# Performance work log

Hardware: AMD Instinct MI355X
Metric: run time of the kernel (lower is better)

The kernel has to match this reference:

```python
import jax, jax.numpy as jnp
import numpy as np

B, NE, NMAX = 256, 90, 270
ZE = PE = GE = PPS = 32
NPROPS = 20
FP, SGE, LATH = 256, 64, 128
PIN = FP + SGE + LATH  # 448 = pred_inp_size = conv input (add_to_node)
C1, C2, H = 448, 256, 3
P1 = P2 = 512
EPS = 1e-5

PNAMES = ['sg_emb_table','lat_W1','lat_b1','lat_bn1_g','lat_bn1_b','lat_bn1_m','lat_bn1_v',
          'lat_W2','lat_b2','lat_bn2_g','lat_bn2_b','lat_bn2_m','lat_bn2_v',
          'z_emb_table','period_table','group_table','props','W_props','b_props','W_phys','b_phys',
          'gat1_W','gat1_as','gat1_ad','gat1_b','gat2_W','gat2_as','gat2_ad','gat2_b',
          'pW1','pb1','pbn1_g','pbn1_b','pbn1_m','pbn1_v',
          'pW2','pb2','pbn2_g','pbn2_b','pbn2_m','pbn2_v','pW3','pb3']

def _bn(x, g, b, m, v):
    return (x - m) * g / jnp.sqrt(v + EPS) + b

def _lrelu(x, s=0.2):
    return jnp.where(x >= 0, x, s * x)

def _gat(x, adj, W, a_s, a_d, bias):
    # PyG DenseGATConv: concat=False (mean over heads), dropout=0, negative_slope=0.2
    Bn, N, _ = x.shape
    h = (x @ W).reshape(Bn, N, H, -1)                      # [B,N,H,C]
    asrc = (h * a_s).sum(-1)                               # [B,N,H]
    adst = (h * a_d).sum(-1)
    alpha = asrc[:, None, :, :] + adst[:, :, None, :]      # [B,i,j,H]
    alpha = _lrelu(alpha, 0.2)
    adj_sl = jnp.maximum(adj, jnp.eye(N, dtype=adj.dtype))  # add self loops
    alpha = jnp.where(adj_sl[..., None] > 0, alpha, -jnp.inf)
    alpha = jax.nn.softmax(alpha, axis=2)                  # softmax over sources j
    out = jnp.einsum('bijh,bjhc->bihc', alpha, h)
    return out.mean(2) + bias                              # [B,N,C]

def _forward(comp, sg, lat, period_idx, group_idx, p):
    sg_x = p['sg_emb_table'][sg[:, 0]]                     # [B,SGE]
    # lattice MLP: (Linear -> BN -> LeakyReLU(True)==identity) x2
    h = _bn(lat @ p['lat_W1'] + p['lat_b1'], p['lat_bn1_g'], p['lat_bn1_b'], p['lat_bn1_m'], p['lat_bn1_v'])
    lat_x = _bn(h @ p['lat_W2'] + p['lat_b2'], p['lat_bn2_g'], p['lat_bn2_b'], p['lat_bn2_m'], p['lat_bn2_v'])
    # ragged -> dense batch: expand composition counts into dense node-type grid
    n_atoms = comp.sum(1)                                  # [B]
    cum = jnp.cumsum(comp, axis=1)                         # [B,NE]
    t = jnp.arange(NMAX)
    z = jax.vmap(lambda c: jnp.searchsorted(c, t, side='right'))(cum)  # [B,NMAX]
    mask = t[None, :] < n_atoms[:, None]                   # [B,NMAX] valid nodes
    z = jnp.where(mask, z, 0)
    # PhysEmbedding: z/period/group embeddings + projected properties -> final proj
    phys = jnp.concatenate([
        p['z_emb_table'][z],
        p['period_table'][period_idx[z]],
        p['group_table'][group_idx[z]],
        p['props'][z] @ p['W_props'] + p['b_props'],
    ], axis=-1)
    phys = phys @ p['W_phys'] + p['b_phys']                # [B,NMAX,FP]
    # add_to_node: cat graph-level lat/sg embeddings onto every node, then zero-pad
    node = jnp.concatenate([
        phys,
        jnp.broadcast_to(lat_x[:, None, :], (lat_x.shape[0], NMAX, LATH)),
        jnp.broadcast_to(sg_x[:, None, :], (sg_x.shape[0], NMAX, SGE)),
    ], axis=-1)
    node = node * mask[..., None].astype(node.dtype)       # to_dense_batch zero padding
    # per-graph dense block adjacency, zero diagonal (fill_diagonal_(0))
    adj = (mask[:, :, None] & mask[:, None, :]).astype(node.dtype)
    adj = adj * (1.0 - jnp.eye(NMAX, dtype=node.dtype))
    # GNNBlock: act = LeakyReLU(True) == identity (negative_slope=1)
    x1 = _gat(node, adj, p['gat1_W'], p['gat1_as'], p['gat1_ad'], p['gat1_b'])
    x2 = _gat(x1, adj, p['gat2_W'], p['gat2_as'], p['gat2_ad'], p['gat2_b'])
    comp_x = x2.sum(1)                                     # sum over ALL NMAX slots (incl. padding, as torch does)
    feat = jnp.concatenate([comp_x, sg_x, lat_x], axis=-1) # [B,PIN]
    # prediction head (eval: dropout off, BN running stats)
    h = _lrelu(_bn(feat @ p['pW1'] + p['pb1'], p['pbn1_g'], p['pbn1_b'], p['pbn1_m'], p['pbn1_v']))
    h = _lrelu(_bn(h @ p['pW2'] + p['pb2'], p['pbn2_g'], p['pbn2_b'], p['pbn2_m'], p['pbn2_v']))
    return h @ p['pW3'] + p['pb3']                         # [B,1]

def setup_inputs():
    key = jax.random.key(0)
    ks = iter(jax.random.split(key, 64))
    def nrm(shape, s=0.05):
        return jax.random.normal(next(ks), shape, dtype=jnp.float32) * s
    comp = jax.random.randint(next(ks), (B, NE), 0, 4, dtype=jnp.int32)
    comp = comp.at[0].set(3)  # graph 0 has exactly NMAX atoms -> data N_max == NMAX
    sg = jax.random.randint(next(ks), (B, 1), 0, 230)
    lat = jax.random.uniform(next(ks), (B, 6), dtype=jnp.float32)
    period_idx = jax.random.randint(next(ks), (NE,), 0, 8)
    group_idx = jax.random.randint(next(ks), (NE,), 0, 19)
    inp = dict(comp=comp, sg=sg, lat=lat, period_idx=period_idx, group_idx=group_idx)
    inp.update(
        sg_emb_table=nrm((230, SGE)),
        lat_W1=nrm((6, LATH)), lat_b1=nrm((LATH,)),
        lat_bn1_g=jnp.ones(LATH), lat_bn1_b=jnp.zeros(LATH), lat_bn1_m=jnp.zeros(LATH), lat_bn1_v=jnp.ones(LATH),
        lat_W2=nrm((LATH, LATH)), lat_b2=nrm((LATH,)),
        lat_bn2_g=jnp.ones(LATH), lat_bn2_b=jnp.zeros(LATH), lat_bn2_m=jnp.zeros(LATH), lat_bn2_v=jnp.ones(LATH),
        z_emb_table=nrm((NE, ZE)), period_table=nrm((8, PE)), group_table=nrm((19, GE)),
        props=nrm((NE, NPROPS), 0.1), W_props=nrm((NPROPS, PPS)), b_props=nrm((PPS,)),
        W_phys=nrm((ZE + PE + GE + PPS, FP)), b_phys=nrm((FP,)),
        gat1_W=nrm((PIN, H * C1)), gat1_as=nrm((H, C1)), gat1_ad=nrm((H, C1)), gat1_b=nrm((C1,)),
        gat2_W=nrm((C1, H * C2)), gat2_as=nrm((H, C2)), gat2_ad=nrm((H, C2)), gat2_b=nrm((C2,)),
        pW1=nrm((PIN, P1)), pb1=nrm((P1,)),
        pbn1_g=jnp.ones(P1), pbn1_b=jnp.zeros(P1), pbn1_m=jnp.zeros(P1), pbn1_v=jnp.ones(P1),
        pW2=nrm((P1, P2)), pb2=nrm((P2,)),
        pbn2_g=jnp.ones(P2), pbn2_b=jnp.zeros(P2), pbn2_m=jnp.zeros(P2), pbn2_v=jnp.ones(P2),
        pW3=nrm((P2, 1)), pb3=nrm((1,)),
    )
    return inp

def reference(comp, sg, lat, period_idx, group_idx,
              sg_emb_table, lat_W1, lat_b1, lat_bn1_g, lat_bn1_b, lat_bn1_m, lat_bn1_v,
              lat_W2, lat_b2, lat_bn2_g, lat_bn2_b, lat_bn2_m, lat_bn2_v,
              z_emb_table, period_table, group_table, props, W_props, b_props, W_phys, b_phys,
              gat1_W, gat1_as, gat1_ad, gat1_b, gat2_W, gat2_as, gat2_ad, gat2_b,
              pW1, pb1, pbn1_g, pbn1_b, pbn1_m, pbn1_v,
              pW2, pb2, pbn2_g, pbn2_b, pbn2_m, pbn2_v, pW3, pb3):
    vals = (sg_emb_table, lat_W1, lat_b1, lat_bn1_g, lat_bn1_b, lat_bn1_m, lat_bn1_v,
            lat_W2, lat_b2, lat_bn2_g, lat_bn2_b, lat_bn2_m, lat_bn2_v,
            z_emb_table, period_table, group_table, props, W_props, b_props, W_phys, b_phys,
            gat1_W, gat1_as, gat1_ad, gat1_b, gat2_W, gat2_as, gat2_ad, gat2_b,
            pW1, pb1, pbn1_g, pbn1_b, pbn1_m, pbn1_v,
            pW2, pb2, pbn2_g, pbn2_b, pbn2_m, pbn2_v, pW3, pb3)
    p = dict(zip(PNAMES, vals))
    return _forward(comp, sg, lat, period_idx, group_idx, p)
```

## Files before the change

### kernel.cpp

```cpp
#include <hip/hip_runtime.h>
#include <math.h>

#define BB 256
#define NEL 90
#define NMAX 270
#define C1 448
#define C2 256
#define PIN 448
#define LATH 128
#define SGE 64
#define P1 512
#define EPSB 1e-5f

typedef short shortx8 __attribute__((ext_vector_type(8)));
typedef float floatx4 __attribute__((ext_vector_type(4)));

__device__ __forceinline__ float bf2f(unsigned short u) {
  return __uint_as_float(((unsigned)u) << 16);
}
__device__ __forceinline__ unsigned short f2bf(float f) {
  unsigned x = __float_as_uint(f);
  unsigned r = (x + 0x7fffu + ((x >> 16) & 1u)) >> 16;
  return (unsigned short)r;
}
__device__ __forceinline__ void gld16(const void* g, void* l) {
  __builtin_amdgcn_global_load_lds(
      (const __attribute__((address_space(1))) unsigned int*)g,
      (__attribute__((address_space(3))) unsigned int*)l, 16, 0, 0);
}

__global__ __launch_bounds__(256) void k_prep(
    const int* __restrict__ comp, const int* __restrict__ sg, const float* __restrict__ lat,
    const float* __restrict__ sg_emb,
    const float* __restrict__ W1, const float* __restrict__ b1,
    const float* __restrict__ g1, const float* __restrict__ be1,
    const float* __restrict__ m1, const float* __restrict__ v1,
    const float* __restrict__ W2, const float* __restrict__ b2,
    const float* __restrict__ g2, const float* __restrict__ be2,
    const float* __restrict__ m2, const float* __restrict__ v2,
    float* __restrict__ sgx, float* __restrict__ latx,
    int* __restrict__ z, int* __restrict__ natoms) {
  int b = blockIdx.x;
  int tid = threadIdx.x;
  __shared__ int cum[NEL];
  __shared__ float hbuf[LATH];
  __shared__ float latl[6];
  if (tid == 0) {
    int s = 0;
    for (int e = 0; e < NEL; ++e) { s += comp[b * NEL + e]; cum[e] = s; }
    natoms[b] = s;
  }
  if (tid < 6) latl[tid] = lat[b * 6 + tid];
  __syncthreads();
  int n = cum[NEL - 1];
  for (int t = tid; t < NMAX; t += blockDim.x) {
    int zz = -1;
    if (t < n) {
      for (int e = 0; e < NEL; ++e) { if (cum[e] > t) { zz = e; break; } }
    }
    z[b * NMAX + t] = zz;
  }
  if (tid < SGE) {
    int si = sg[b];
    sgx[b * SGE + tid] = sg_emb[si * SGE + tid];
  }
  if (tid < LATH) {
    float acc = b1[tid];
    for (int k = 0; k < 6; ++k) acc += latl[k] * W1[k * LATH + tid];
    acc = (acc - m1[tid]) * g1[tid] * rsqrtf(v1[tid] + EPSB) + be1[tid];
    hbuf[tid] = acc;
  }
  __syncthreads();
  if (tid < LATH) {
    float acc = b2[tid];
    for (int k = 0; k < LATH; ++k) acc += hbuf[k] * W2[k * LATH + tid];
    acc = (acc - m2[tid]) * g2[tid] * rsqrtf(v2[tid] + EPSB) + be2[tid];
    latx[b * LATH + tid] = acc;
  }
}

__global__ __launch_bounds__(256) void k_scan(const int* __restrict__ natoms,
                                              int* __restrict__ off,
                                              int* __restrict__ aoff,
                                              float* __restrict__ zerobuf) {
  __shared__ int sh[BB];
  int tid = threadIdx.x;
  zerobuf[tid] = 0.f;
  int v0 = natoms[tid];
  sh[tid] = v0;
  for (int d = 1; d < BB; d <<= 1) {
    __syncthreads();
    int v = (tid >= d) ? sh[tid - d] : 0;
    __syncthreads();
    sh[tid] += v;
  }
  __syncthreads();
  off[tid] = sh[tid] - v0;
  __syncthreads();
  int sz = 3 * ((((v0 + 15) >> 4) << 4)) * ((((v0 + 31) >> 5) << 5));
  sh[tid] = sz;
  for (int d = 1; d < BB; d <<= 1) {
    __syncthreads();
    int v = (tid >= d) ? sh[tid - d] : 0;
    __syncthreads();
    sh[tid] += v;
  }
  __syncthreads();
  aoff[tid] = sh[tid] - sz;
}

__global__ __launch_bounds__(256) void k_physpe(
    const int* __restrict__ period_idx, const int* __restrict__ group_idx,
    const float* __restrict__ z_emb, const float* __restrict__ period_t,
    const float* __restrict__ group_t, const float* __restrict__ props,
    const float* __restrict__ Wp, const float* __restrict__ bp,
    const float* __restrict__ Wphys, const float* __restrict__ bphys,
    float* __restrict__ physpe) {
  int e = blockIdx.x;
  int tid = threadIdx.x;
  __shared__ float ph[128];
  if (tid < 32) ph[tid] = z_emb[e * 32 + tid];
  else if (tid < 64) ph[tid] = period_t[period_idx[e] * 32 + tid - 32];
  else if (tid < 96) ph[tid] = group_t[group_idx[e] * 32 + tid - 64];
  else if (tid < 128) {
    int j = tid - 96;
    float acc = bp[j];
    for (int k = 0; k < 20; ++k) acc += props[e * 20 + k] * Wp[k * 32 + j];
    ph[tid] = acc;
  }
  __syncthreads();
  float acc = bphys[tid];
  for (int k = 0; k < 128; ++k) acc += ph[k] * Wphys[k * 256 + tid];
  physpe[e * 256 + tid] = acc;
}

__global__ __launch_bounds__(256) void k_nodep(
    const int* __restrict__ z, const int* __restrict__ off, const int* __restrict__ natoms,
    const float* __restrict__ physpe, const float* __restrict__ latx,
    const float* __restrict__ sgx, unsigned short* __restrict__ x0) {
  int b = blockIdx.x;
  int n = natoms[b], ob = off[b];
  int tid = threadIdx.x;
  __shared__ int zl[NMAX];
  for (int t = tid; t < n; t += 256) zl[t] = z[b * NMAX + t];
  __syncthreads();
  int items = n * 56;
  for (int e = tid; e < items; e += 256) {
    int t = e / 56, c8 = (e - t * 56) << 3;
    int zt = zl[t];
    float v[8];
    if (c8 < 256) {
      float4 a = *(const float4*)(physpe + zt * 256 + c8);
      float4 c = *(const float4*)(physpe + zt * 256 + c8 + 4);
      v[0] = a.x; v[1] = a.y; v[2] = a.z; v[3] = a.w;
      v[4] = c.x; v[5] = c.y; v[6] = c.z; v[7] = c.w;
    } else if (c8 < 384) {
      float4 a = *(const float4*)(latx + b * LATH + c8 - 256);
      float4 c = *(const float4*)(latx + b * LATH + c8 - 252);
      v[0] = a.x; v[1] = a.y; v[2] = a.z; v[3] = a.w;
      v[4] = c.x; v[5] = c.y; v[6] = c.z; v[7] = c.w;
    } else {
      float4 a = *(const float4*)(sgx + b * SGE + c8 - 384);
      float4 c = *(const float4*)(sgx + b * SGE + c8 - 380);
      v[0] = a.x; v[1] = a.y; v[2] = a.z; v[3] = a.w;
      v[4] = c.x; v[5] = c.y; v[6] = c.z; v[7] = c.w;
    }
    unsigned short u[8];
    #pragma unroll
    for (int i = 0; i < 8; ++i) u[i] = f2bf(v[i]);
    *(uint4*)(x0 + (size_t)(ob + t) * PIN + c8) = *(uint4*)u;
  }
}

__global__ __launch_bounds__(256) void k_wprep(
    const float* __restrict__ W, unsigned short* __restrict__ Wt, int K, int NC3) {
  int k0 = blockIdx.x << 5;
  int c0 = blockIdx.y << 5;
  __shared__ float ts[32][33];
  int e = threadIdx.x << 2;
  int kk = e >> 5, cc = e & 31;
  float4 v = *(const float4*)(W + (size_t)(k0 + kk) * NC3 + c0 + cc);
  ts[kk][cc] = v.x; ts[kk][cc + 1] = v.y; ts[kk][cc + 2] = v.z; ts[kk][cc + 3] = v.w;
  __syncthreads();
  int c2 = threadIdx.x & 31, kg = threadIdx.x >> 5;
  ushort4 u;
  u.x = f2bf(ts[kg * 4 + 0][c2]); u.y = f2bf(ts[kg * 4 + 1][c2]);
  u.z = f2bf(ts[kg * 4 + 2][c2]); u.w = f2bf(ts[kg * 4 + 3][c2]);
  *(ushort4*)(Wt + (size_t)(c0 + c2) * K + k0 + (kg << 2)) = u;
}

__global__ __launch_bounds__(64) void k_fold(
    const float* __restrict__ W, const float* __restrict__ a_s, const float* __restrict__ a_d,
    int NC3, int C, float* __restrict__ wsv, float* __restrict__ wdv) {
  int k = blockIdx.x;
  int tid = threadIdx.x;
  for (int h = 0; h < 3; ++h) {
    float ss = 0.f, sd = 0.f;
    for (int c = tid; c < C; c += 64) {
      float wv = W[(size_t)k * NC3 + h * C + c];
      ss += wv * a_s[h * C + c];
      sd += wv * a_d[h * C + c];
    }
    for (int o = 32; o > 0; o >>= 1) { ss += __shfl_down(ss, o); sd += __shfl_down(sd, o); }
    if (tid == 0) { wsv[k * 3 + h] = ss; wdv[k * 3 + h] = sd; }
  }
}

__global__ __launch_bounds__(256) void k_av2(
    const unsigned short* __restrict__ x, const float* __restrict__ wsv,
    const float* __restrict__ wdv, const int* __restrict__ off,
    const int* __restrict__ natoms, float* __restrict__ asrc,
    float* __restrict__ adst, int K) {
  __shared__ float sw[C1 * 3], dw[C1 * 3];
  int tid = threadIdx.x;
  for (int e = tid; e < K * 3; e += 256) { sw[e] = wsv[e]; dw[e] = wdv[e]; }
  __syncthreads();
  int total = off[BB - 1] + natoms[BB - 1];
  int row = blockIdx.x * 256 + tid;
  if (row >= total) return;
  const unsigned short* xr = x + (size_t)row * K;
  float s0 = 0.f, s1 = 0.f, s2 = 0.f, d0 = 0.f, d1 = 0.f, d2 = 0.f;
  for (int k = 0; k < K; k += 8) {
    uint4 raw = *(const uint4*)(xr + k);
    unsigned short us[8];
    *(uint4*)us = raw;
    #pragma unroll
    for (int u = 0; u < 8; ++u) {
      float xv = bf2f(us[u]);
      int kb = (k + u) * 3;
      s0 += xv * sw[kb + 0]; s1 += xv * sw[kb + 1]; s2 += xv * sw[kb + 2];
      d0 += xv * dw[kb + 0]; d1 += xv * dw[kb + 1]; d2 += xv * dw[kb + 2];
    }
  }
  asrc[row * 3 + 0] = s0; asrc[row * 3 + 1] = s1; asrc[row * 3 + 2] = s2;
  adst[row * 3 + 0] = d0; adst[row * 3 + 1] = d1; adst[row * 3 + 2] = d2;
}

#define MTMAX 17
__global__ __launch_bounds__(256) void k_alpha(
    const float* __restrict__ asrc, const float* __restrict__ adst,
    const int* __restrict__ off, const int* __restrict__ natoms,
    const int* __restrict__ aoff, unsigned short* __restrict__ alpha) {
  int bid = blockIdx.x;
  int b = bid & (BB - 1);
  int hm = bid >> 8;
  int h = hm % 3;
  int mt = hm / 3;
  int n = natoms[b];
  if (n == 0) return;
  int mtn = (n + 15) >> 4;
  if (mt >= mtn) return;
  int ktn = (n + 31) >> 5;
  int rext = mtn << 4, kext = ktn << 5;
  int ob = off[b];
  size_t ab = (size_t)aoff[b] + (size_t)h * rext * kext;
  int tid = threadIdx.x;
  int wv = tid >> 6, lane = tid & 63;
  __shared__ float asl[288];
  for (int j = tid; j < kext; j += 256)
    asl[j] = (j < n) ? asrc[(ob + j) * 3 + h] : 0.f;
  __syncthreads();
  #pragma unroll
  for (int r = 0; r < 4; ++r) {
    int i = (mt << 4) + (wv << 2) + r;
    unsigned short* rowp = alpha + ab + (size_t)i * kext;
    if (i >= n) {
      for (int j = lane; j < kext; j += 64) rowp[j] = 0;
      continue;
    }
    float ad = adst[(ob + i) * 3 + h];
    float m = -1e30f;
    for (int j = lane; j < n; j += 64) {
      float sc = asl[j] + ad;
      sc = fmaxf(sc, 0.2f * sc);
      m = fmaxf(m, sc);
    }
    for (int o = 32; o > 0; o >>= 1) m = fmaxf(m, __shfl_xor(m, o));
    float s = 0.f;
    for (int j = lane; j < n; j += 64) {
      float sc = asl[j] + ad;
      sc = fmaxf(sc, 0.2f * sc);
      s += __expf(sc - m);
    }
    for (int o = 32; o > 0; o >>= 1) s += __shfl_xor(s, o);
    float rs = 1.f / s;
    for (int j = lane; j < kext; j += 64) {
      float v = 0.f;
      if (j < n) {
        float sc = asl[j] + ad;
        sc = fmaxf(sc, 0.2f * sc);
        v = __expf(sc - m) * rs;
      }
      rowp[j] = f2bf(v);
    }
  }
}

#define MTW 5

__global__ __launch_bounds__(256, 2) void k_fused_mfma(
    const unsigned short* __restrict__ xin, const unsigned short* __restrict__ Wt,
    const unsigned short* __restrict__ alpha, const int* __restrict__ aoff,
    const int* __restrict__ off, const int* __restrict__ natoms,
    const float* __restrict__ bias, const float* __restrict__ zerobuf,
    unsigned short* __restrict__ xout, int K, int C, int NC) {
  int bid = blockIdx.x;
  int xg = bid & 7;
  int g = bid >> 3;
  int cblk = g % NC;
  int b = xg + ((g / NC) << 3);
  int c0 = cblk << 6;
  int n = natoms[b];
  if (n == 0) return;
  int ob = off[b];
  size_t ab = (size_t)aoff[b];
  int tid = threadIdx.x;
  int wv = tid >> 6;
  int lane = tid & 63;
  int m16 = lane & 15;
  int q = lane >> 4;

  int mtn = (n + 15) >> 4;
  int jmax = mtn << 4;
  int ktn = (n + 31) >> 5;
  int kext = ktn << 5;
  size_t hstride = (size_t)jmax * kext;

  __shared__ unsigned short xs[2][17 * 512];
  __shared__ unsigned short tt[36 * 512];

  const unsigned short* xsrc[MTW];
  #pragma unroll
  for (int t_i = 0; t_i < MTW; ++t_i) {
    int mt = wv + (t_i << 2);
    int j = (mt << 4) + m16;
    xsrc[t_i] = (j < n) ? (xin + (size_t)(ob + j) * K + (q << 3))
                        : (const unsigned short*)zerobuf;
  }

  floatx4 acc[MTW][4];
  #pragma unroll
  for (int i = 0; i < MTW; ++i)
    #pragma unroll
    for (int nt = 0; nt < 4; ++nt) acc[i][nt] = (floatx4)0.f;

  for (int h = 0; h < 3; ++h) {
    floatx4 tac[MTW][4];
    #pragma unroll
    for (int i = 0; i < MTW; ++i)
      #pragma unroll
      for (int nt = 0; nt < 4; ++nt) tac[i][nt] = (floatx4)0.f;

    const unsigned short* wsrc = Wt + (size_t)(h * C + c0 + lane) * K + (wv << 3);

    #pragma unroll
    for (int t_i = 0; t_i < MTW; ++t_i) {
      int mt = wv + (t_i << 2);
      if (mt < mtn) gld16(xsrc[t_i], &xs[0][mt << 9]);
    }
    gld16(wsrc, &tt[wv << 9]);
    __syncthreads();

    int buf = 0;
    for (int k0 = 0; k0 < K; k0 += 32) {
      int k1 = k0 + 32;
      if (k1 < K) {
        #pragma unroll
        for (int t_i = 0; t_i < MTW; ++t_i) {
          int mt = wv + (t_i << 2);
          if (mt < mtn) gld16(xsrc[t_i] + k1, &xs[buf ^ 1][mt << 9]);
        }
        gld16(wsrc + k1, &tt[((buf ^ 1) << 11) + (wv << 9)]);
      }
      const unsigned short* wb = &tt[buf << 11];
      shortx8 bfr[4];
      #pragma unroll
      for (int nt = 0; nt < 4; ++nt)
        bfr[nt] = *(const shortx8*)(wb + (q << 9) + (((nt << 4) + m16) << 3));
      #pragma unroll
      for (int t_i = 0; t_i < MTW; ++t_i) {
        int mt = wv + (t_i << 2);
        if (mt < mtn) {
          shortx8 a = *(const shortx8*)(&xs[buf][(mt << 9) + (((q << 4) + m16) << 3)]);
          #pragma unroll
          for (int nt = 0; nt < 4; ++nt)
            tac[t_i][nt] = __builtin_amdgcn_mfma_f32_16x16x32_bf16(a, bfr[nt], tac[t_i][nt], 0, 0, 0);
        }
      }
      __syncthreads();
      buf ^= 1;
    }
    #pragma unroll
    for (int t_i = 0; t_i < MTW; ++t_i) {
      int mt = wv + (t_i << 2);
      if (mt < mtn) {
        int jbase = (mt << 4) + (q << 2);
        #pragma unroll
        for (int nt = 0; nt < 4; ++nt) {
          floatx4 d = tac[t_i][nt];
          ushort4 u;
          u.x = f2bf(d.x); u.y = f2bf(d.y); u.z = f2bf(d.z); u.w = f2bf(d.w);
          int c = (nt << 4) + m16;
          *(ushort4*)(tt + ((jbase >> 3) << 9) + (c << 3) + (jbase & 7)) = u;
        }
      }
    }
    for (int e = tid; e < ((kext - jmax) << 6); e += 256) {
      int j = jmax + (e >> 6), c = e & 63;
      tt[((j >> 3) << 9) + (c << 3) + (j & 7)] = 0;
    }
    __syncthreads();
    const unsigned short* ap = alpha + ab + (size_t)h * hstride;
    for (int k0p = 0; k0p < kext; k0p += 32) {
      shortx8 tb[4];
      #pragma unroll
      for (int nt = 0; nt < 4; ++nt)
        tb[nt] = *(const shortx8*)(tt + (((k0p >> 3) + q) << 9) + (((nt << 4) + m16) << 3));
      #pragma unroll
      for (int t_i = 0; t_i < MTW; ++t_i) {
        int mt = wv + (t_i << 2);
        if (mt < mtn) {
          shortx8 af = *(const shortx8*)(ap + (size_t)((mt << 4) + m16) * kext + k0p + (q << 3));
          #pragma unroll
          for (int nt = 0; nt < 4; ++nt)
            acc[t_i][nt] = __builtin_amdgcn_mfma_f32_16x16x32_bf16(af, tb[nt], acc[t_i][nt], 0, 0, 0);
        }
      }
    }
    __syncthreads();
  }
  float bq[4];
  #pragma unroll
  for (int nt = 0; nt < 4; ++nt) bq[nt] = bias[c0 + (nt << 4) + m16];
  const float inv3 = 1.f / 3.f;
  #pragma unroll
  for (int t_i = 0; t_i < MTW; ++t_i) {
    int mt = wv + (t_i << 2);
    if (mt < mtn) {
      #pragma unroll
      for (int nt = 0; nt < 4; ++nt) {
        floatx4 d = acc[t_i][nt];
        int cidx = c0 + (nt << 4) + m16;
        #pragma unroll
        for (int r = 0; r < 4; ++r) {
          int i = (mt << 4) + (q << 2) + r;
          if (i < n) xout[(size_t)(ob + i) * C + cidx] = f2bf(d[r] * inv3 + bq[nt]);
        }
      }
    }
  }
}

__global__ __launch_bounds__(128) void k_pad(
    const float* __restrict__ b1, const float* __restrict__ W2,
    const float* __restrict__ b2g, float* __restrict__ pad2) {
  int c = blockIdx.x;
  int tid = threadIdx.x;
  float s = 0.f;
  for (int k = tid; k < C1; k += 128) {
    float bv = b1[k];
    const float* wr = W2 + (size_t)k * (3 * C2) + c;
    s += bv * (wr[0] + wr[C2] + wr[2 * C2]);
  }
  __shared__ float red[128];
  red[tid] = s;
  __syncthreads();
  for (int st = 64; st > 0; st >>= 1) {
    if (tid < st) red[tid] += red[tid + st];
    __syncthreads();
  }
  if (tid == 0) pad2[c] = red[0] * (1.f / 3.f) + b2g[c];
}

__global__ __launch_bounds__(256) void k_feat2(
    const unsigned short* __restrict__ x2, const float* __restrict__ pad2,
    const int* __restrict__ off, const int* __restrict__ natoms,
    const float* __restrict__ sgx, const float* __restrict__ latx,
    float* __restrict__ feat) {
  int b = blockIdx.y;
  int chunk = blockIdx.x;
  int tid = threadIdx.x;
  int n = natoms[b], ob = off[b];
  if (chunk == 17) {
    atomicAdd(&feat[b * PIN + tid], (float)(NMAX - n) * pad2[tid]);
    if (tid < SGE) feat[b * PIN + 256 + tid] = sgx[b * SGE + tid];
    if (tid < LATH) feat[b * PIN + 320 + tid] = latx[b * LATH + tid];
    return;
  }
  int i0 = chunk << 4;
  if (i0 >= n) return;
  int i1 = min(i0 + 16, n);
  float s = 0.f;
  for (int i = i0; i < i1; ++i) s += bf2f(x2[(size_t)(ob + i) * C2 + tid]);
  atomicAdd(&feat[b * PIN + tid], s);
}

__global__ __launch_bounds__(512) void k_head(
    const float* __restrict__ feat,
    const float* __restrict__ W1, const float* __restrict__ b1,
    const float* __restrict__ g1, const float* __restrict__ be1,
    const float* __restrict__ m1, const float* __restrict__ v1,
    const float* __restrict__ W2, const float* __restrict__ b2,
    const float* __restrict__ g2, const float* __restrict__ be2,
    const float* __restrict__ m2, const float* __restrict__ v2,
    const float* __restrict__ W3, const float* __restrict__ b3,
    float* __restrict__ out) {
  int b = blockIdx.x, tid = threadIdx.x;
  __shared__ float f[PIN];
  __shared__ float h1[P1];
  __shared__ float h2[P1];
  __shared__ float red[512];
  for (int i = tid; i < PIN; i += 512) f[i] = feat[b * PIN + i];
  __syncthreads();
  {
    int o = tid;
    float acc = b1[o];
    for (int k = 0; k < PIN; ++k) acc += f[k] * W1[k * P1 + o];
    acc = (acc - m1[o]) * g1[o] * rsqrtf(v1[o] + EPSB) + be1[o];
    h1[o] = acc >= 0.f ? acc : 0.2f * acc;
  }
  __syncthreads();
  {
    int o = tid;
    float acc = b2[o];
    for (int k = 0; k < P1; ++k) acc += h1[k] * W2[k * P1 + o];
    acc = (acc - m2[o]) * g2[o] * rsqrtf(v2[o] + EPSB) + be2[o];
    h2[o] = acc >= 0.f ? acc : 0.2f * acc;
  }
  __syncthreads();
  red[tid] = h2[tid] * W3[tid];
  __syncthreads();
  for (int s = 256; s > 0; s >>= 1) {
    if (tid < s) red[tid] += red[tid + s];
    __syncthreads();
  }
  if (tid == 0) out[b] = red[0] + b3[0];
}

extern "C" void kernel_launch(void* const* d_in, const int* in_sizes, int n_in,
                              void* d_out, int out_size, void* d_ws, size_t ws_size,
                              hipStream_t stream) {
  const int*   comp       = (const int*)d_in[0];
  const int*   sg         = (const int*)d_in[1];
  const float* lat        = (const float*)d_in[2];
  const int*   period_idx = (const int*)d_in[3];
  const int*   group_idx  = (const int*)d_in[4];
  const float* sg_emb     = (const float*)d_in[5];
  const float* lat_W1     = (const float*)d_in[6];
  const float* lat_b1     = (const float*)d_in[7];
  const float* lat_bn1_g  = (const float*)d_in[8];
  const float* lat_bn1_b  = (const float*)d_in[9];
  const float* lat_bn1_m  = (const float*)d_in[10];
  const float* lat_bn1_v  = (const float*)d_in[11];
  const float* lat_W2     = (const float*)d_in[12];
  const float* lat_b2     = (const float*)d_in[13];
  const float* lat_bn2_g  = (const float*)d_in[14];
  const float* lat_bn2_b  = (const float*)d_in[15];
  const float* lat_bn2_m  = (const float*)d_in[16];
  const float* lat_bn2_v  = (const float*)d_in[17];
  const float* z_emb      = (const float*)d_in[18];
  const float* period_t   = (const float*)d_in[19];
  const float* group_t    = (const float*)d_in[20];
  const float* props      = (const float*)d_in[21];
  const float* W_props    = (const float*)d_in[22];
  const float* b_props    = (const float*)d_in[23];
  const float* W_phys     = (const float*)d_in[24];
  const float* b_phys     = (const float*)d_in[25];
  const float* gat1_W     = (const float*)d_in[26];
  const float* gat1_as    = (const float*)d_in[27];
  const float* gat1_ad    = (const float*)d_in[28];
  const float* gat1_b     = (const float*)d_in[29];
  const float* gat2_W     = (const float*)d_in[30];
  const float* gat2_as    = (const float*)d_in[31];
  const float* gat2_ad    = (const float*)d_in[32];
  const float* gat2_b     = (const float*)d_in[33];
  const float* pW1        = (const float*)d_in[34];
  const float* pb1        = (const float*)d_in[35];
  const float* pbn1_g     = (const float*)d_in[36];
  const float* pbn1_b     = (const float*)d_in[37];
  const float* pbn1_m     = (const float*)d_in[38];
  const float* pbn1_v     = (const float*)d_in[39];
  const float* pW2        = (const float*)d_in[40];
  const float* pb2        = (const float*)d_in[41];
  const float* pbn2_g     = (const float*)d_in[42];
  const float* pbn2_b     = (const float*)d_in[43];
  const float* pbn2_m     = (const float*)d_in[44];
  const float* pbn2_v     = (const float*)d_in[45];
  const float* pW3        = (const float*)d_in[46];
  const float* pb3        = (const float*)d_in[47];

  float* ws = (float*)d_ws;
  const size_t o_sgx  = 0;
  const size_t o_latx = o_sgx  + (size_t)BB * SGE;
  const size_t o_nat  = o_latx + (size_t)BB * LATH;
  const size_t o_off  = o_nat  + BB;
  const size_t o_aoff = o_off  + BB;
  const size_t o_z    = o_aoff + BB;
  const size_t o_phys = o_z    + (size_t)BB * NMAX;
  const size_t o_wsv  = o_phys + (size_t)NEL * 256;
  const size_t o_wdv  = o_wsv  + (size_t)C1 * 3;
  const size_t o_asrc = o_wdv  + (size_t)C1 * 3;
  const size_t o_adst = o_asrc + (size_t)BB * NMAX * 3;
  const size_t o_pad2 = o_adst + (size_t)BB * NMAX * 3;
  const size_t o_zero = o_pad2 + 256;
  const size_t o_wt1  = o_zero + 256;
  const size_t o_wt2  = o_wt1  + (size_t)(3 * C1) * PIN / 2;
  const size_t o_x0   = o_wt2  + (size_t)(3 * C2) * C1 / 2;
  const size_t o_x1   = o_x0   + (size_t)BB * NMAX * PIN / 2;
  const size_t o_alph = o_x1   + (size_t)BB * NMAX * PIN / 2;

  float* sgx    = ws + o_sgx;
  float* latx   = ws + o_latx;
  int*   natoms = (int*)(ws + o_nat);
  int*   off    = (int*)(ws + o_off);
  int*   aoff   = (int*)(ws + o_aoff);
  int*   z      = (int*)(ws + o_z);
  float* physpe = ws + o_phys;
  float* wsv    = ws + o_wsv;
  float* wdv    = ws + o_wdv;
  float* asrc   = ws + o_asrc;
  float* adst   = ws + o_adst;
  float* pad2   = ws + o_pad2;
  float* zerobuf = ws + o_zero;
  unsigned short* wt1   = (unsigned short*)(ws + o_wt1);
  unsigned short* wt2   = (unsigned short*)(ws + o_wt2);
  unsigned short* x0    = (unsigned short*)(ws + o_x0);
  unsigned short* x1    = (unsigned short*)(ws + o_x1);
  unsigned short* x2    = x0;
  unsigned short* alpha = (unsigned short*)(ws + o_alph);
  float* feat   = ws + o_x1;

  const int AVG = (BB * NMAX + 255) / 256;
  const int ALG = BB * 3 * MTMAX;

  k_prep<<<BB, 256, 0, stream>>>(comp, sg, lat, sg_emb,
      lat_W1, lat_b1, lat_bn1_g, lat_bn1_b, lat_bn1_m, lat_bn1_v,
      lat_W2, lat_b2, lat_bn2_g, lat_bn2_b, lat_bn2_m, lat_bn2_v,
      sgx, latx, z, natoms);
  k_scan<<<1, 256, 0, stream>>>(natoms, off, aoff, zerobuf);
  k_physpe<<<NEL, 256, 0, stream>>>(period_idx, group_idx, z_emb, period_t, group_t,
      props, W_props, b_props, W_phys, b_phys, physpe);
  k_nodep<<<BB, 256, 0, stream>>>(z, off, natoms, physpe, latx, sgx, x0);

  k_wprep<<<dim3(PIN / 32, (3 * C1) / 32), 256, 0, stream>>>(gat1_W, wt1, PIN, 3 * C1);
  k_wprep<<<dim3(C1 / 32, (3 * C2) / 32), 256, 0, stream>>>(gat2_W, wt2, C1, 3 * C2);
  k_pad<<<256, 128, 0, stream>>>(gat1_b, gat2_W, gat2_b, pad2);

  k_fold<<<C1, 64, 0, stream>>>(gat1_W, gat1_as, gat1_ad, 3 * C1, C1, wsv, wdv);
  k_av2<<<AVG, 256, 0, stream>>>(x0, wsv, wdv, off, natoms, asrc, adst, PIN);
  k_alpha<<<ALG, 256, 0, stream>>>(asrc, adst, off, natoms, aoff, alpha);
  k_fused_mfma<<<(C1 / 64) * BB, 256, 0, stream>>>(x0, wt1, alpha, aoff,
      off, natoms, gat1_b, zerobuf, x1, PIN, C1, C1 / 64);

  k_fold<<<C1, 64, 0, stream>>>(gat2_W, gat2_as, gat2_ad, 3 * C2, C2, wsv, wdv);
  k_av2<<<AVG, 256, 0, stream>>>(x1, wsv, wdv, off, natoms, asrc, adst, C1);
  k_alpha<<<ALG, 256, 0, stream>>>(asrc, adst, off, natoms, aoff, alpha);
  k_fused_mfma<<<(C2 / 64) * BB, 256, 0, stream>>>(x1, wt2, alpha, aoff,
      off, natoms, gat2_b, zerobuf, x2, C1, C2, C2 / 64);

  hipMemsetAsync(feat, 0, (size_t)BB * PIN * sizeof(float), stream);
  k_feat2<<<dim3(18, BB), 256, 0, stream>>>(x2, pad2, off, natoms, sgx, latx, feat);
  k_head<<<BB, 512, 0, stream>>>(feat,
      pW1, pb1, pbn1_g, pbn1_b, pbn1_m, pbn1_v,
      pW2, pb2, pbn2_g, pbn2_b, pbn2_m, pbn2_v,
      pW3, pb3, (float*)d_out);
}
```

Baseline: 753.6 us.

## Halve GAT column tile and read GEMM operands directly from global memory

The fused GAT kernel now computes 32 output columns per block instead of 64, doubling the grid and shrinking the LDS transpose buffer. The first GEMM stage drops the double-buffered global-to-LDS staging and its per-step barriers, loading X rows and weight fragments straight into registers. Occupancy hint rises from 2 to 3 blocks per CU. The aim is more parallelism and fewer syncs, at the cost of more redundant global reads of X and alpha across column blocks and less load/compute overlap.

```diff
diff --git a/kernel.cpp b/kernel.cpp
--- a/kernel.cpp
+++ b/kernel.cpp
@@ -11,6 +11,7 @@
 #define SGE 64
 #define P1 512
 #define EPSB 1e-5f
+#define KDIM 448
 
 typedef short shortx8 __attribute__((ext_vector_type(8)));
 typedef float floatx4 __attribute__((ext_vector_type(4)));
@@ -22,11 +23,6 @@
   unsigned x = __float_as_uint(f);
   unsigned r = (x + 0x7fffu + ((x >> 16) & 1u)) >> 16;
   return (unsigned short)r;
-}
-__device__ __forceinline__ void gld16(const void* g, void* l) {
-  __builtin_amdgcn_global_load_lds(
-      (const __attribute__((address_space(1))) unsigned int*)g,
-      (__attribute__((address_space(3))) unsigned int*)l, 16, 0, 0);
 }
 
 __global__ __launch_bounds__(256) void k_prep(
@@ -298,18 +294,18 @@
 
 #define MTW 5
 
-__global__ __launch_bounds__(256, 2) void k_fused_mfma(
+__global__ __launch_bounds__(256, 3) void k_fused_mfma(
     const unsigned short* __restrict__ xin, const unsigned short* __restrict__ Wt,
     const unsigned short* __restrict__ alpha, const int* __restrict__ aoff,
     const int* __restrict__ off, const int* __restrict__ natoms,
     const float* __restrict__ bias, const float* __restrict__ zerobuf,
-    unsigned short* __restrict__ xout, int K, int C, int NC) {
+    unsigned short* __restrict__ xout, int C, int NC) {
   int bid = blockIdx.x;
   int xg = bid & 7;
   int g = bid >> 3;
   int cblk = g % NC;
   int b = xg + ((g / NC) << 3);
-  int c0 = cblk << 6;
+  int c0 = cblk << 5;
   int n = natoms[b];
   if (n == 0) return;
   int ob = off[b];
@@ -326,69 +322,42 @@
   int kext = ktn << 5;
   size_t hstride = (size_t)jmax * kext;
 
-  __shared__ unsigned short xs[2][17 * 512];
-  __shared__ unsigned short tt[36 * 512];
+  __shared__ unsigned short tt[36 * 256];
 
   const unsigned short* xsrc[MTW];
   #pragma unroll
   for (int t_i = 0; t_i < MTW; ++t_i) {
     int mt = wv + (t_i << 2);
     int j = (mt << 4) + m16;
-    xsrc[t_i] = (j < n) ? (xin + (size_t)(ob + j) * K + (q << 3))
+    xsrc[t_i] = (j < n) ? (xin + (size_t)(ob + j) * KDIM + (q << 3))
                         : (const unsigned short*)zerobuf;
   }
 
-  floatx4 acc[MTW][4];
+  floatx4 acc[MTW][2];
   #pragma unroll
-  for (int i = 0; i < MTW; ++i)
+  for (int i = 0; i < MTW; ++i) { acc[i][0] = (floatx4)0.f; acc[i][1] = (floatx4)0.f; }
+
+  for (int h = 0; h < 3; ++h) {
+    floatx4 tac[MTW][2];
     #pragma unroll
-    for (int nt = 0; nt < 4; ++nt) acc[i][nt] = (floatx4)0.f;
-
-  for (int h = 0; h < 3; ++h) {
-    floatx4 tac[MTW][4];
-    #pragma unroll
-    for (int i = 0; i < MTW; ++i)
-      #pragma unroll
-      for (int nt = 0; nt < 4; ++nt) tac[i][nt] = (floatx4)0.f;
-
-    const unsigned short* wsrc = Wt + (size_t)(h * C + c0 + lane) * K + (wv << 3);
-
-    #pragma unroll
-    for (int t_i = 0; t_i < MTW; ++t_i) {
-      int mt = wv + (t_i << 2);
-      if (mt < mtn) gld16(xsrc[t_i], &xs[0][mt << 9]);
-    }
-    gld16(wsrc, &tt[wv << 9]);
-    __syncthreads();
-
-    int buf = 0;
-    for (int k0 = 0; k0 < K; k0 += 32) {
-      int k1 = k0 + 32;
-      if (k1 < K) {
-        #pragma unroll
-        for (int t_i = 0; t_i < MTW; ++t_i) {
-          int mt = wv + (t_i << 2);
-          if (mt < mtn) gld16(xsrc[t_i] + k1, &xs[buf ^ 1][mt << 9]);
-        }
-        gld16(wsrc + k1, &tt[((buf ^ 1) << 11) + (wv << 9)]);
-      }
-      const unsigned short* wb = &tt[buf << 11];
-      shortx8 bfr[4];
-      #pragma unroll
-      for (int nt = 0; nt < 4; ++nt)
-        bfr[nt] = *(const shortx8*)(wb + (q << 9) + (((nt << 4) + m16) << 3));
+    for (int i = 0; i < MTW; ++i) { tac[i][0] = (floatx4)0.f; tac[i][1] = (floatx4)0.f; }
+
+    const unsigned short* wp0 = Wt + (size_t)(h * C + c0 + m16) * KDIM + (q << 3);
+    const unsigned short* wp1 = Wt + (size_t)(h * C + c0 + 16 + m16) * KDIM + (q << 3);
+
+    #pragma unroll 2
+    for (int k0 = 0; k0 < KDIM; k0 += 32) {
+      shortx8 b0 = *(const shortx8*)(wp0 + k0);
+      shortx8 b1 = *(const shortx8*)(wp1 + k0);
       #pragma unroll
       for (int t_i = 0; t_i < MTW; ++t_i) {
         int mt = wv + (t_i << 2);
         if (mt < mtn) {
-          shortx8 a = *(const shortx8*)(&xs[buf][(mt << 9) + (((q << 4) + m16) << 3)]);
-          #pragma unroll
-          for (int nt = 0; nt < 4; ++nt)
-            tac[t_i][nt] = __builtin_amdgcn_mfma_f32_16x16x32_bf16(a, bfr[nt], tac[t_i][nt], 0, 0, 0);
+          shortx8 a = *(const shortx8*)(xsrc[t_i] + k0);
+          tac[t_i][0] = __builtin_amdgcn_mfma_f32_16x16x32_bf16(a, b0, tac[t_i][0], 0, 0, 0);
+          tac[t_i][1] = __builtin_amdgcn_mfma_f32_16x16x32_bf16(a, b1, tac[t_i][1], 0, 0, 0);
         }
       }
-      __syncthreads();
-      buf ^= 1;
     }
     #pragma unroll
     for (int t_i = 0; t_i < MTW; ++t_i) {
@@ -396,55 +365,52 @@
       if (mt < mtn) {
         int jbase = (mt << 4) + (q << 2);
         #pragma unroll
-        for (int nt = 0; nt < 4; ++nt) {
+        for (int nt = 0; nt < 2; ++nt) {
           floatx4 d = tac[t_i][nt];
           ushort4 u;
           u.x = f2bf(d.x); u.y = f2bf(d.y); u.z = f2bf(d.z); u.w = f2bf(d.w);
           int c = (nt << 4) + m16;
-          *(ushort4*)(tt + ((jbase >> 3) << 9) + (c << 3) + (jbase & 7)) = u;
+          *(ushort4*)(tt + ((jbase >> 3) << 8) + (c << 3) + (jbase & 7)) = u;
         }
       }
     }
-    for (int e = tid; e < ((kext - jmax) << 6); e += 256) {
-      int j = jmax + (e >> 6), c = e & 63;
-      tt[((j >> 3) << 9) + (c << 3) + (j & 7)] = 0;
+    for (int e = tid; e < ((kext - jmax) << 5); e += 256) {
+      int j = jmax + (e >> 5), c = e & 31;
+      tt[((j >> 3) << 8) + (c << 3) + (j & 7)] = 0;
     }
     __syncthreads();
     const unsigned short* ap = alpha + ab + (size_t)h * hstride;
     for (int k0p = 0; k0p < kext; k0p += 32) {
-      shortx8 tb[4];
-      #pragma unroll
-      for (int nt = 0; nt < 4; ++nt)
-        tb[nt] = *(const shortx8*)(tt + (((k0p >> 3) + q) << 9) + (((nt << 4) + m16) << 3));
+      shortx8 tb0 = *(const shortx8*)(tt + (((k0p >> 3) + q) << 8) + (m16 << 3));
+      shortx8 tb1 = *(const shortx8*)(tt + (((k0p >> 3) + q) << 8) + ((16 + m16) << 3));
       #pragma unroll
       for (int t_i = 0; t_i < MTW; ++t_i) {
         int mt = wv + (t_i << 2);
         if (mt < mtn) {
           shortx8 af = *(const shortx8*)(ap + (size_t)((mt << 4) + m16) * kext + k0p + (q << 3));
-          #pragma unroll
-          for (int nt = 0; nt < 4; ++nt)
-            acc[t_i][nt] = __builtin_amdgcn_mfma_f32_16x16x32_bf16(af, tb[nt], acc[t_i][nt], 0, 0, 0);
+          acc[t_i][0] = __builtin_amdgcn_mfma_f32_16x16x32_bf16(af, tb0, acc[t_i][0], 0, 0, 0);
+          acc[t_i][1] = __builtin_amdgcn_mfma_f32_16x16x32_bf16(af, tb1, acc[t_i][1], 0, 0, 0);
         }
       }
     }
     __syncthreads();
   }
-  float bq[4];
-  #pragma unroll
-  for (int nt = 0; nt < 4; ++nt) bq[nt] = bias[c0 + (nt << 4) + m16];
+  float bq0 = bias[c0 + m16];
+  float bq1 = bias[c0 + 16 + m16];
   const float inv3 = 1.f / 3.f;
   #pragma unroll
   for (int t_i = 0; t_i < MTW; ++t_i) {
     int mt = wv + (t_i << 2);
     if (mt < mtn) {
       #pragma unroll
-      for (int nt = 0; nt < 4; ++nt) {
+      for (int nt = 0; nt < 2; ++nt) {
         floatx4 d = acc[t_i][nt];
+        float bq = nt ? bq1 : bq0;
         int cidx = c0 + (nt << 4) + m16;
         #pragma unroll
         for (int r = 0; r < 4; ++r) {
           int i = (mt << 4) + (q << 2) + r;
-          if (i < n) xout[(size_t)(ob + i) * C + cidx] = f2bf(d[r] * inv3 + bq[nt]);
+          if (i < n) xout[(size_t)(ob + i) * C + cidx] = f2bf(d[r] * inv3 + bq);
         }
       }
     }
@@ -649,14 +615,14 @@
   k_fold<<<C1, 64, 0, stream>>>(gat1_W, gat1_as, gat1_ad, 3 * C1, C1, wsv, wdv);
   k_av2<<<AVG, 256, 0, stream>>>(x0, wsv, wdv, off, natoms, asrc, adst, PIN);
   k_alpha<<<ALG, 256, 0, stream>>>(asrc, adst, off, natoms, aoff, alpha);
-  k_fused_mfma<<<(C1 / 64) * BB, 256, 0, stream>>>(x0, wt1, alpha, aoff,
-      off, natoms, gat1_b, zerobuf, x1, PIN, C1, C1 / 64);
+  k_fused_mfma<<<(C1 / 32) * BB, 256, 0, stream>>>(x0, wt1, alpha, aoff,
+      off, natoms, gat1_b, zerobuf, x1, C1, C1 / 32);
 
   k_fold<<<C1, 64, 0, stream>>>(gat2_W, gat2_as, gat2_ad, 3 * C2, C2, wsv, wdv);
   k_av2<<<AVG, 256, 0, stream>>>(x1, wsv, wdv, off, natoms, asrc, adst, C1);
   k_alpha<<<ALG, 256, 0, stream>>>(asrc, adst, off, natoms, aoff, alpha);
-  k_fused_mfma<<<(C2 / 64) * BB, 256, 0, stream>>>(x1, wt2, alpha, aoff,
-      off, natoms, gat2_b, zerobuf, x2, C1, C2, C2 / 64);
+  k_fused_mfma<<<(C2 / 32) * BB, 256, 0, stream>>>(x1, wt2, alpha, aoff,
+      off, natoms, gat2_b, zerobuf, x2, C2, C2 / 32);
 
   hipMemsetAsync(feat, 0, (size_t)BB * PIN * sizeof(float), stream);
   k_feat2<<<dim3(18, BB), 256, 0, stream>>>(x2, pad2, off, natoms, sgx, latx, feat);
```

Measured after the change: 991.9 us. 31.6% more time.
